# Performance work log

Measured on AMD Instinct MI355X. Metric: run time of the kernel, lower is better.

## Reference

```python
import jax, jax.numpy as jnp
import numpy as np

N = 20000   # nodes
E = 320000  # edges
D_IN = 256
D_OUT = 256


def setup_inputs() -> dict:
    key = jax.random.key(0)
    ks = jax.random.split(key, 12)
    s = 0.05
    return {
        "h": jax.random.normal(ks[0], (N, D_OUT), jnp.float32),
        "x": jax.random.normal(ks[1], (N, D_IN), jnp.float32),
        "pos": jax.random.normal(ks[2], (N, 3), jnp.float32),
        "W_fc": jax.random.normal(ks[3], (D_OUT, D_IN + D_OUT), jnp.float32) * s,
        "b_fc": jax.random.normal(ks[4], (D_OUT,), jnp.float32) * s,
        "W_conv": jax.random.normal(ks[5], (D_OUT, D_OUT), jnp.float32) * s,
        "W_ih": jax.random.normal(ks[6], (3 * D_OUT, D_OUT), jnp.float32) * s,
        "W_hh": jax.random.normal(ks[7], (3 * D_OUT, D_OUT), jnp.float32) * s,
        "b_ih": jax.random.normal(ks[8], (3 * D_OUT,), jnp.float32) * s,
        "b_hh": jax.random.normal(ks[9], (3 * D_OUT,), jnp.float32) * s,
        "edge_index_gate": jax.random.randint(ks[10], (2, E), 0, N, jnp.int64),
        "edge_index_cand": jax.random.randint(ks[11], (2, E), 0, N, jnp.int64),
    }


def reference(h, x, pos, W_fc, b_fc, W_conv, W_ih, W_hh, b_ih, b_hh,
              edge_index_gate, edge_index_cand):
    # fc + relu on concatenated [x, h]
    xh = jnp.concatenate([x, h], axis=-1)            # [N, in+out]
    xr = jax.nn.relu(xh @ W_fc.T + b_fc)             # [N, out]

    # GatedGraphConv, num_layers=1, aggr='add'
    m = xr @ W_conv                                  # [N, out]  (x @ weight[0])
    src, dst = edge_index_gate[0], edge_index_gate[1]
    agg = jax.ops.segment_sum(m[src], dst, num_segments=xr.shape[0])  # [N, out]

    # GRUCell(agg, xr)  (torch semantics: input=agg, hidden=xr)
    gi = agg @ W_ih.T + b_ih                         # [N, 3*out]
    gh = xr @ W_hh.T + b_hh                          # [N, 3*out]
    i_r, i_z, i_n = jnp.split(gi, 3, axis=-1)
    h_r, h_z, h_n = jnp.split(gh, 3, axis=-1)
    r = jax.nn.sigmoid(i_r + h_r)
    z = jax.nn.sigmoid(i_z + h_z)
    n = jnp.tanh(i_n + r * h_n)
    h_next = (1.0 - z) * n + z * xr
    return h_next
```

## Files before the change

kernel.cpp:

```cpp
#include <hip/hip_runtime.h>
#include <hip/hip_bf16.h>

#define N_NODES 20000
#define MPAD 20032
#define CAP 64

typedef __attribute__((ext_vector_type(8))) short short8;
typedef __attribute__((ext_vector_type(4))) float f32x4;

#define MFMA16(a,b,c) __builtin_amdgcn_mfma_f32_16x16x32_bf16(a,b,c,0,0,0)

#define FSW(r) (((r) & 3) ^ (((r) >> 2) & 3))

#define WAIT_BAR(NSTR) do { \
  asm volatile("s_waitcnt vmcnt(" NSTR ") lgkmcnt(0)" ::: "memory"); \
  __builtin_amdgcn_s_barrier(); \
  __builtin_amdgcn_sched_barrier(0); \
} while (0)
#define END_BAR() do { \
  __builtin_amdgcn_sched_barrier(0); \
  __builtin_amdgcn_s_barrier(); \
} while (0)

static __device__ __forceinline__ ushort f2bf(float f) {
  union { float f; uint u; } v; v.f = f;
  uint u = v.u;
  uint r = (u + 0x7FFFu + ((u >> 16) & 1u)) >> 16;
  return (ushort)r;
}
static __device__ __forceinline__ float bf2f(ushort s) {
  union { uint u; float f; } v; v.u = ((uint)s) << 16; return v.f;
}

typedef __attribute__((address_space(1))) const unsigned int guint;
typedef __attribute__((address_space(3))) unsigned int luint;
static __device__ __forceinline__ void gl2lds16(const void* g, void* l) {
  __builtin_amdgcn_global_load_lds((guint*)g, (luint*)l, 16, 0, 0);
}

static __device__ __forceinline__ void cvt8(const float* __restrict__ s, ushort* __restrict__ d) {
  float4 v0 = *(const float4*)s;
  float4 v1 = *(const float4*)(s + 4);
  union { ushort u[8]; uint4 v; } t;
  t.u[0]=f2bf(v0.x); t.u[1]=f2bf(v0.y); t.u[2]=f2bf(v0.z); t.u[3]=f2bf(v0.w);
  t.u[4]=f2bf(v1.x); t.u[5]=f2bf(v1.y); t.u[6]=f2bf(v1.z); t.u[7]=f2bf(v1.w);
  *(uint4*)d = t.v;
}
static __device__ __forceinline__ void cvt8_lds(const float* __restrict__ s, ushort* d) {
  float4 v0 = *(const float4*)s;
  float4 v1 = *(const float4*)(s + 4);
  union { ushort u[8]; uint4 v; } t;
  t.u[0]=f2bf(v0.x); t.u[1]=f2bf(v0.y); t.u[2]=f2bf(v0.z); t.u[3]=f2bf(v0.w);
  t.u[4]=f2bf(v1.x); t.u[5]=f2bf(v1.y); t.u[6]=f2bf(v1.z); t.u[7]=f2bf(v1.w);
  *(uint4*)d = t.v;
}

__global__ __launch_bounds__(256, 4) void k_mid(
    const float* __restrict__ x, const float* __restrict__ h,
    const float* __restrict__ Wfc, const float* __restrict__ bfc,
    ushort* __restrict__ AX,
    const float* __restrict__ Wih, const float* __restrict__ Wc,
    const float* __restrict__ Whh, ushort* __restrict__ Bg3,
    const int* __restrict__ eg, int* __restrict__ cnt, int* __restrict__ srcs) {
  __shared__ __attribute__((aligned(16))) ushort smem[8192];
  int bid = blockIdx.x;
  int t = threadIdx.x, w = t >> 6, l = t & 63;

  if (bid >= 1400) {
    int e = (bid - 1400) * 256 + t;
    if (e < 320000) {
      int d = eg[320000 + e];
      int slot = atomicAdd(&cnt[d], 1);
      if (slot < CAP) srcs[d * CAP + slot] = eg[e];
    }
    return;
  }

  if (bid >= 1304) {
    int i = (bid - 1304) * 256 + t;
    int row = i >> 5;
    int k0 = (i & 31) * 8;
    int g = row / 48, rem = row - g * 48;
    int p = rem >> 4, ci = rem & 15;
    int c = g * 16 + ci;
    cvt8(Whh + ((size_t)(p * 256 + c)) * 256 + k0, Bg3 + (size_t)row * 512 + 256 + k0);
    return;
  }

  if (bid >= 1256) {
    ushort* sA = smem;
    ushort* sB = smem + 2048;
    int wf = bid - 1256;
    int row0 = (wf % 12) * 64, col0 = (wf / 12) * 64;
    int wr = (w >> 1) * 32, wc = (w & 1) * 32;
    f32x4 acc[2][2] = {};
    for (int ks = 0; ks < 8; ++ks) {
      int k0 = ks * 32;
      {
        int r = t >> 2, wl = t & 3;
        int gw = wl ^ FSW(r);
        cvt8_lds(Wih + (size_t)(row0 + r) * 256 + k0 + gw * 8, &sA[r*32 + wl*8]);
        cvt8_lds(Wc  + (size_t)(col0 + r) * 256 + k0 + gw * 8, &sB[r*32 + wl*8]);
      }
      __syncthreads();
      short8 af[2], bfr[2];
      #pragma unroll
      for (int mi = 0; mi < 2; ++mi) {
        int r = wr + mi * 16 + (l & 15);
        af[mi] = *(short8*)&sA[r * 32 + (((l >> 4)) ^ FSW(r)) * 8];
      }
      #pragma unroll
      for (int ni = 0; ni < 2; ++ni) {
        int br = wc + ni * 16 + (l & 15);
        bfr[ni] = *(short8*)&sB[br * 32 + (((l >> 4)) ^ FSW(br)) * 8];
      }
      #pragma unroll
      for (int mi = 0; mi < 2; ++mi)
        #pragma unroll
        for (int ni = 0; ni < 2; ++ni)
          acc[mi][ni] = MFMA16(af[mi], bfr[ni], acc[mi][ni]);
      __syncthreads();
    }
    #pragma unroll
    for (int mi = 0; mi < 2; ++mi)
      #pragma unroll
      for (int ni = 0; ni < 2; ++ni)
        #pragma unroll
        for (int q = 0; q < 4; ++q) {
          int jj = row0 + wr + mi*16 + (l>>4)*4 + q;
          int tc = col0 + wc + ni*16 + (l&15);
          int p = jj >> 8, c = jj & 255;
          int brow = (c >> 4) * 48 + p * 16 + (c & 15);
          Bg3[(size_t)brow * 512 + tc] = f2bf(acc[mi][ni][q]);
        }
    return;
  }

  ushort* sA = smem;
  ushort* sB = smem + 4096;
  int wk = (bid & 7) * 157 + (bid >> 3);
  int panel = wk >> 2, ch = wk & 3;
  if (panel >= 313) return;
  int row0 = panel * 64, col0 = ch * 64;
  int wr = (w >> 1) * 32, wc = (w & 1) * 32;

  f32x4 acc[2][2] = {};
  for (int ks = 0; ks < 8; ++ks) {
    int k0 = ks * 64;
    const float* Af = (ks < 4) ? x : h;
    int ka = k0 & 255;
    #pragma unroll
    for (int j = 0; j < 2; ++j) {
      int ci = t + j * 256;
      int r = ci >> 3, wl = ci & 7;
      int gw = wl ^ (r & 7);
      int gr = row0 + r; if (gr > N_NODES - 1) gr = N_NODES - 1;
      cvt8_lds(Af + (size_t)gr * 256 + ka + gw * 8, &sA[r*64 + wl*8]);
    }
    #pragma unroll
    for (int j = 0; j < 2; ++j) {
      int ci = t + j * 256;
      int r = ci >> 3, wl = ci & 7;
      int gw = wl ^ (r & 7);
      cvt8_lds(Wfc + (size_t)(col0 + r) * 512 + k0 + gw * 8, &sB[r*64 + wl*8]);
    }
    __syncthreads();
    #pragma unroll
    for (int j = 0; j < 2; ++j) {
      short8 af[2], bfr[2];
      #pragma unroll
      for (int mi = 0; mi < 2; ++mi) {
        int r = wr + mi * 16 + (l & 15);
        af[mi] = *(short8*)&sA[r * 64 + ((j * 4 + (l >> 4)) ^ (r & 7)) * 8];
      }
      #pragma unroll
      for (int ni = 0; ni < 2; ++ni) {
        int br = wc + ni * 16 + (l & 15);
        bfr[ni] = *(short8*)&sB[br * 64 + ((j * 4 + (l >> 4)) ^ (br & 7)) * 8];
      }
      #pragma unroll
      for (int mi = 0; mi < 2; ++mi)
        #pragma unroll
        for (int ni = 0; ni < 2; ++ni)
          acc[mi][ni] = MFMA16(af[mi], bfr[ni], acc[mi][ni]);
    }
    __syncthreads();
  }
  #pragma unroll
  for (int mi = 0; mi < 2; ++mi)
    #pragma unroll
    for (int ni = 0; ni < 2; ++ni)
      #pragma unroll
      for (int q = 0; q < 4; ++q) {
        int r = row0 + wr + mi*16 + (l>>4)*4 + q;
        int c = col0 + wc + ni*16 + (l&15);
        if (r < N_NODES) {
          float v = acc[mi][ni][q] + bfc[c];
          v = v > 0.f ? v : 0.f;
          AX[(size_t)r * 512 + 256 + c] = f2bf(v);
        }
      }
}

__global__ __launch_bounds__(256) void k_aggS(
    const int* __restrict__ cnt, const int* __restrict__ srcs,
    ushort* __restrict__ AX) {
  int node = blockIdx.x * 8 + (threadIdx.x >> 5);
  if (node >= N_NODES) return;
  int lane = threadIdx.x & 31;
  const int* bkt = srcs + node * CAP;
  int n = cnt[node]; if (n > CAP) n = CAP;
  float a[8] = {};
  int i = 0;
  for (; i + 4 <= n; i += 4) {
    uint4 v0 = *(const uint4*)(AX + (size_t)bkt[i  ] * 512 + 256 + lane * 8);
    uint4 v1 = *(const uint4*)(AX + (size_t)bkt[i+1] * 512 + 256 + lane * 8);
    uint4 v2 = *(const uint4*)(AX + (size_t)bkt[i+2] * 512 + 256 + lane * 8);
    uint4 v3 = *(const uint4*)(AX + (size_t)bkt[i+3] * 512 + 256 + lane * 8);
    const ushort* p0 = (const ushort*)&v0; const ushort* p1 = (const ushort*)&v1;
    const ushort* p2 = (const ushort*)&v2; const ushort* p3 = (const ushort*)&v3;
    #pragma unroll
    for (int j = 0; j < 8; j++) a[j] += (bf2f(p0[j]) + bf2f(p1[j])) + (bf2f(p2[j]) + bf2f(p3[j]));
  }
  for (; i < n; ++i) {
    uint4 v0 = *(const uint4*)(AX + (size_t)bkt[i] * 512 + 256 + lane * 8);
    const ushort* p0 = (const ushort*)&v0;
    #pragma unroll
    for (int j = 0; j < 8; j++) a[j] += bf2f(p0[j]);
  }
  union { ushort s[8]; uint4 v; } o;
  #pragma unroll
  for (int j = 0; j < 8; j++) o.s[j] = f2bf(a[j]);
  *(uint4*)(AX + (size_t)node * 512 + lane * 8) = o.v;
}

static __device__ __forceinline__ void gru3_stage(
    const ushort* __restrict__ AX, const ushort* __restrict__ Bg3,
    ushort* sA, ushort* sB, int row0, int bro, int w, int l, int ks) {
  int k0 = ks * 64;
  #pragma unroll
  for (int j = 0; j < 2; ++j) {
    int rb = w * 16 + j * 8;
    int r = rb + (l >> 3);
    int gw = (l & 7) ^ (r & 7);
    gl2lds16(AX + (size_t)(row0 + r) * 512 + k0 + gw * 8, (char*)sA + (size_t)rb * 128);
  }
  #pragma unroll
  for (int j = 0; j < 6; ++j) {
    int rb = j * 32 + w * 8;
    int r = rb + (l >> 3);
    int gw = (l & 7) ^ (r & 7);
    gl2lds16(Bg3 + (size_t)(bro + r) * 512 + k0 + gw * 8, (char*)sB + (size_t)rb * 128);
  }
}

template<int PN>
static __device__ __forceinline__ void gru3_compute(
    const ushort* sA, const ushort* sB, int w, int l, f32x4 (&acc)[4][4]) {
  __builtin_amdgcn_s_setprio(1);
  #pragma unroll
  for (int j = 0; j < 2; ++j) {
    short8 af[4], bfr[3];
    #pragma unroll
    for (int mi = 0; mi < 4; ++mi) {
      int r = mi * 16 + (l & 15);
      af[mi] = *(const short8*)&sA[r * 64 + ((j * 4 + (l >> 4)) ^ (r & 7)) * 8];
    }
    #pragma unroll
    for (int p = 0; p < 3; ++p) {
      int br = w * 48 + p * 16 + (l & 15);
      bfr[p] = *(const short8*)&sB[br * 64 + ((j * 4 + (l >> 4)) ^ (br & 7)) * 8];
    }
    #pragma unroll
    for (int mi = 0; mi < 4; ++mi) {
      acc[mi][0]  = MFMA16(af[mi], bfr[0], acc[mi][0]);
      acc[mi][1]  = MFMA16(af[mi], bfr[1], acc[mi][1]);
      acc[mi][PN] = MFMA16(af[mi], bfr[2], acc[mi][PN]);
    }
  }
  __builtin_amdgcn_s_setprio(0);
}

__global__ __launch_bounds__(256, 2) void k_gru3(
    const ushort* __restrict__ AX, const ushort* __restrict__ Bg3,
    const float* __restrict__ bih, const float* __restrict__ bhh,
    float* __restrict__ out) {
  __shared__ __attribute__((aligned(16))) ushort smem[2 * 16384];
  ushort* sA0 = smem;
  ushort* sB0 = smem + 4096;
  ushort* sA1 = smem + 16384;
  ushort* sB1 = smem + 20480;
  int bid = blockIdx.x;
  int wk = (bid & 7) * 157 + (bid >> 3);
  int panel = wk >> 2, ch = wk & 3;
  if (panel >= 313) return;
  int row0 = panel * 64;
  int bro = ch * 192;
  int t = threadIdx.x, w = t >> 6, l = t & 63;

  gru3_stage(AX, Bg3, sA0, sB0, row0, bro, w, l, 0);
  __syncthreads();

  f32x4 acc[4][4] = {};
  #pragma unroll
  for (int ks = 0; ks < 8; ++ks) {
    ushort* cA = (ks & 1) ? sA1 : sA0;
    ushort* cB = (ks & 1) ? sB1 : sB0;
    ushort* nA = (ks & 1) ? sA0 : sA1;
    ushort* nB = (ks & 1) ? sB0 : sB1;
    if (ks < 7) gru3_stage(AX, Bg3, nA, nB, row0, bro, w, l, ks + 1);
    if (ks < 7) WAIT_BAR("8");
    else        WAIT_BAR("0");
    if (ks < 4) gru3_compute<2>(cA, cB, w, l, acc);
    else        gru3_compute<3>(cA, cB, w, l, acc);
    END_BAR();
  }

  int c = ch * 64 + w * 16 + (l & 15);
  float br_ = bih[c] + bhh[c];
  float bz_ = bih[256 + c] + bhh[256 + c];
  float bi_ = bih[512 + c];
  float bh_ = bhh[512 + c];
  #pragma unroll
  for (int mi = 0; mi < 4; ++mi)
    #pragma unroll
    for (int q = 0; q < 4; ++q) {
      int r = row0 + mi*16 + (l>>4)*4 + q;
      if (r < N_NODES) {
        float rg = 1.f / (1.f + __expf(-(acc[mi][0][q] + br_)));
        float zg = 1.f / (1.f + __expf(-(acc[mi][1][q] + bz_)));
        float ng = tanhf((acc[mi][2][q] + bi_) + rg * (acc[mi][3][q] + bh_));
        float xv = bf2f(AX[(size_t)r * 512 + 256 + c]);
        out[(size_t)r * 256 + c] = (1.f - zg) * ng + zg * xv;
      }
    }
}

extern "C" void kernel_launch(void* const* d_in, const int* in_sizes, int n_in,
                              void* d_out, int out_size, void* d_ws, size_t ws_size,
                              hipStream_t stream) {
  const float* h   = (const float*)d_in[0];
  const float* x   = (const float*)d_in[1];
  const float* Wfc = (const float*)d_in[3];
  const float* bfc = (const float*)d_in[4];
  const float* Wc  = (const float*)d_in[5];
  const float* Wih = (const float*)d_in[6];
  const float* Whh = (const float*)d_in[7];
  const float* bih = (const float*)d_in[8];
  const float* bhh = (const float*)d_in[9];
  const int*   eg  = (const int*)d_in[10];
  float* out = (float*)d_out;

  char* ws = (char*)d_ws;
  ushort* AX   = (ushort*)(ws);
  ushort* Bg3  = (ushort*)(ws + 20512768);
  int*    cnt    = (int*)(ws + 21299200);
  int*    srcs   = (int*)(ws + 21379200);

  hipMemsetAsync(cnt, 0, (size_t)N_NODES * 4, stream);

  k_mid<<<2650, 256, 0, stream>>>(x, h, Wfc, bfc, AX, Wih, Wc, Whh, Bg3, eg, cnt, srcs);

  k_aggS<<<(N_NODES + 7) / 8, 256, 0, stream>>>(cnt, srcs, AX);

  k_gru3<<<1256, 256, 0, stream>>>(AX, Bg3, bih, bhh, out);
}
```

Baseline: 88.78 us.

## Pre-convert W_fc to bf16 and double-buffer the fc GEMM with wider tiles

A new small kernel converts W_fc to bf16 once, so the fc GEMM can stream B tiles straight into LDS with global_load_lds instead of converting fp32 per block. The fc GEMM tile grows from 64x64 to 64x128 and uses double-buffered LDS: the next A tile is loaded into registers and the next B tile into the other buffer while the current tile's MFMAs run. This halves the number of fc blocks and hides load latency, at the cost of more LDS per block (occupancy hint lowered to 3) and an extra kernel launch.

Measured after the change: 93.32 us. +5.1%, slower.

```diff
diff --git a/kernel.cpp b/kernel.cpp
--- a/kernel.cpp
+++ b/kernel.cpp
@@ -46,28 +46,32 @@
   t.u[4]=f2bf(v1.x); t.u[5]=f2bf(v1.y); t.u[6]=f2bf(v1.z); t.u[7]=f2bf(v1.w);
   *(uint4*)d = t.v;
 }
-static __device__ __forceinline__ void cvt8_lds(const float* __restrict__ s, ushort* d) {
-  float4 v0 = *(const float4*)s;
-  float4 v1 = *(const float4*)(s + 4);
+static __device__ __forceinline__ void pack8(float4 v0, float4 v1, ushort* d) {
   union { ushort u[8]; uint4 v; } t;
   t.u[0]=f2bf(v0.x); t.u[1]=f2bf(v0.y); t.u[2]=f2bf(v0.z); t.u[3]=f2bf(v0.w);
   t.u[4]=f2bf(v1.x); t.u[5]=f2bf(v1.y); t.u[6]=f2bf(v1.z); t.u[7]=f2bf(v1.w);
   *(uint4*)d = t.v;
 }
 
-__global__ __launch_bounds__(256, 4) void k_mid(
+__global__ __launch_bounds__(256) void k_prep0(
+    const float* __restrict__ Wfc, ushort* __restrict__ WfcB) {
+  int i = blockIdx.x * 256 + threadIdx.x;
+  if (i < 16384) cvt8(Wfc + i * 8, WfcB + i * 8);
+}
+
+__global__ __launch_bounds__(256, 3) void k_mid(
     const float* __restrict__ x, const float* __restrict__ h,
-    const float* __restrict__ Wfc, const float* __restrict__ bfc,
+    const ushort* __restrict__ WfcB, const float* __restrict__ bfc,
     ushort* __restrict__ AX,
     const float* __restrict__ Wih, const float* __restrict__ Wc,
     const float* __restrict__ Whh, ushort* __restrict__ Bg3,
     const int* __restrict__ eg, int* __restrict__ cnt, int* __restrict__ srcs) {
-  __shared__ __attribute__((aligned(16))) ushort smem[8192];
+  __shared__ __attribute__((aligned(16))) ushort smem[24576];
   int bid = blockIdx.x;
   int t = threadIdx.x, w = t >> 6, l = t & 63;
 
-  if (bid >= 1400) {
-    int e = (bid - 1400) * 256 + t;
+  if (bid >= 776) {
+    int e = (bid - 776) * 256 + t;
     if (e < 320000) {
       int d = eg[320000 + e];
       int slot = atomicAdd(&cnt[d], 1);
@@ -76,8 +80,8 @@
     return;
   }
 
-  if (bid >= 1304) {
-    int i = (bid - 1304) * 256 + t;
+  if (bid >= 680) {
+    int i = (bid - 680) * 256 + t;
     int row = i >> 5;
     int k0 = (i & 31) * 8;
     int g = row / 48, rem = row - g * 48;
@@ -87,10 +91,10 @@
     return;
   }
 
-  if (bid >= 1256) {
+  if (bid >= 632) {
     ushort* sA = smem;
     ushort* sB = smem + 2048;
-    int wf = bid - 1256;
+    int wf = bid - 632;
     int row0 = (wf % 12) * 64, col0 = (wf / 12) * 64;
     int wr = (w >> 1) * 32, wc = (w & 1) * 32;
     f32x4 acc[2][2] = {};
@@ -99,8 +103,8 @@
       {
         int r = t >> 2, wl = t & 3;
         int gw = wl ^ FSW(r);
-        cvt8_lds(Wih + (size_t)(row0 + r) * 256 + k0 + gw * 8, &sA[r*32 + wl*8]);
-        cvt8_lds(Wc  + (size_t)(col0 + r) * 256 + k0 + gw * 8, &sB[r*32 + wl*8]);
+        cvt8(Wih + (size_t)(row0 + r) * 256 + k0 + gw * 8, &sA[r*32 + wl*8]);
+        cvt8(Wc  + (size_t)(col0 + r) * 256 + k0 + gw * 8, &sB[r*32 + wl*8]);
       }
       __syncthreads();
       short8 af[2], bfr[2];
@@ -136,64 +140,91 @@
     return;
   }
 
-  ushort* sA = smem;
-  ushort* sB = smem + 4096;
-  int wk = (bid & 7) * 157 + (bid >> 3);
-  int panel = wk >> 2, ch = wk & 3;
+  ushort* A0 = smem;
+  ushort* B0 = smem + 4096;
+  ushort* A1 = smem + 12288;
+  ushort* B1 = smem + 16384;
+  int wk = (bid & 7) * 79 + (bid >> 3);
+  int panel = wk >> 1, ch = wk & 1;
   if (panel >= 313) return;
-  int row0 = panel * 64, col0 = ch * 64;
-  int wr = (w >> 1) * 32, wc = (w & 1) * 32;
-
-  f32x4 acc[2][2] = {};
+  int row0 = panel * 64, col0 = ch * 128;
+
+  int r0c = t >> 3,        wl0 = t & 7,        gw0 = wl0 ^ (r0c & 7);
+  int r1c = (t + 256) >> 3, wl1 = t & 7,       gw1 = wl1 ^ (r1c & 7);
+  int gr0 = row0 + r0c; if (gr0 > N_NODES - 1) gr0 = N_NODES - 1;
+  int gr1 = row0 + r1c; if (gr1 > N_NODES - 1) gr1 = N_NODES - 1;
+
+  {
+    const float* Af = x;
+    cvt8(Af + (size_t)gr0 * 256 + 0 + gw0 * 8, &A0[r0c * 64 + wl0 * 8]);
+    cvt8(Af + (size_t)gr1 * 256 + 0 + gw1 * 8, &A0[r1c * 64 + wl1 * 8]);
+    #pragma unroll
+    for (int j = 0; j < 4; ++j) {
+      int rb = j * 32 + w * 8;
+      int r = rb + (l >> 3);
+      int gw = (l & 7) ^ (r & 7);
+      gl2lds16(WfcB + (size_t)(col0 + r) * 512 + 0 + gw * 8, (char*)B0 + (size_t)rb * 128);
+    }
+  }
+  __syncthreads();
+
+  f32x4 acc[4][2] = {};
+  #pragma unroll
   for (int ks = 0; ks < 8; ++ks) {
-    int k0 = ks * 64;
-    const float* Af = (ks < 4) ? x : h;
-    int ka = k0 & 255;
+    ushort* cA = (ks & 1) ? A1 : A0;
+    ushort* cB = (ks & 1) ? B1 : B0;
+    ushort* nA = (ks & 1) ? A0 : A1;
+    ushort* nB = (ks & 1) ? B0 : B1;
+    float4 a0, a1, a2, a3;
+    if (ks < 7) {
+      const float* Af = (ks + 1 < 4) ? x : h;
+      int ka = ((ks + 1) * 64) & 255;
+      const float* pa0 = Af + (size_t)gr0 * 256 + ka + gw0 * 8;
+      const float* pa1 = Af + (size_t)gr1 * 256 + ka + gw1 * 8;
+      a0 = *(const float4*)pa0; a1 = *(const float4*)(pa0 + 4);
+      a2 = *(const float4*)pa1; a3 = *(const float4*)(pa1 + 4);
+      int k0 = (ks + 1) * 64;
+      #pragma unroll
+      for (int j = 0; j < 4; ++j) {
+        int rb = j * 32 + w * 8;
+        int r = rb + (l >> 3);
+        int gw = (l & 7) ^ (r & 7);
+        gl2lds16(WfcB + (size_t)(col0 + r) * 512 + k0 + gw * 8, (char*)nB + (size_t)rb * 128);
+      }
+    }
     #pragma unroll
     for (int j = 0; j < 2; ++j) {
-      int ci = t + j * 256;
-      int r = ci >> 3, wl = ci & 7;
-      int gw = wl ^ (r & 7);
-      int gr = row0 + r; if (gr > N_NODES - 1) gr = N_NODES - 1;
-      cvt8_lds(Af + (size_t)gr * 256 + ka + gw * 8, &sA[r*64 + wl*8]);
-    }
-    #pragma unroll
-    for (int j = 0; j < 2; ++j) {
-      int ci = t + j * 256;
-      int r = ci >> 3, wl = ci & 7;
-      int gw = wl ^ (r & 7);
-      cvt8_lds(Wfc + (size_t)(col0 + r) * 512 + k0 + gw * 8, &sB[r*64 + wl*8]);
-    }
-    __syncthreads();
-    #pragma unroll
-    for (int j = 0; j < 2; ++j) {
-      short8 af[2], bfr[2];
-      #pragma unroll
-      for (int mi = 0; mi < 2; ++mi) {
-        int r = wr + mi * 16 + (l & 15);
-        af[mi] = *(short8*)&sA[r * 64 + ((j * 4 + (l >> 4)) ^ (r & 7)) * 8];
+      short8 af[4], bfr[2];
+      #pragma unroll
+      for (int mi = 0; mi < 4; ++mi) {
+        int r = mi * 16 + (l & 15);
+        af[mi] = *(short8*)&cA[r * 64 + ((j * 4 + (l >> 4)) ^ (r & 7)) * 8];
       }
       #pragma unroll
       for (int ni = 0; ni < 2; ++ni) {
-        int br = wc + ni * 16 + (l & 15);
-        bfr[ni] = *(short8*)&sB[br * 64 + ((j * 4 + (l >> 4)) ^ (br & 7)) * 8];
-      }
-      #pragma unroll
-      for (int mi = 0; mi < 2; ++mi)
+        int br = w * 32 + ni * 16 + (l & 15);
+        bfr[ni] = *(short8*)&cB[br * 64 + ((j * 4 + (l >> 4)) ^ (br & 7)) * 8];
+      }
+      #pragma unroll
+      for (int mi = 0; mi < 4; ++mi)
         #pragma unroll
         for (int ni = 0; ni < 2; ++ni)
           acc[mi][ni] = MFMA16(af[mi], bfr[ni], acc[mi][ni]);
     }
+    if (ks < 7) {
+      pack8(a0, a1, &nA[r0c * 64 + wl0 * 8]);
+      pack8(a2, a3, &nA[r1c * 64 + wl1 * 8]);
+    }
     __syncthreads();
   }
   #pragma unroll
-  for (int mi = 0; mi < 2; ++mi)
+  for (int mi = 0; mi < 4; ++mi)
     #pragma unroll
     for (int ni = 0; ni < 2; ++ni)
       #pragma unroll
       for (int q = 0; q < 4; ++q) {
-        int r = row0 + wr + mi*16 + (l>>4)*4 + q;
-        int c = col0 + wc + ni*16 + (l&15);
+        int r = row0 + mi*16 + (l>>4)*4 + q;
+        int c = col0 + w*32 + ni*16 + (l&15);
         if (r < N_NODES) {
           float v = acc[mi][ni][q] + bfc[c];
           v = v > 0.f ? v : 0.f;
@@ -354,12 +385,14 @@
   char* ws = (char*)d_ws;
   ushort* AX   = (ushort*)(ws);
   ushort* Bg3  = (ushort*)(ws + 20512768);
-  int*    cnt    = (int*)(ws + 21299200);
-  int*    srcs   = (int*)(ws + 21379200);
+  ushort* WfcB = (ushort*)(ws + 21299200);
+  int*    cnt    = (int*)(ws + 21561344);
+  int*    srcs   = (int*)(ws + 21641344);
 
   hipMemsetAsync(cnt, 0, (size_t)N_NODES * 4, stream);
-
-  k_mid<<<2650, 256, 0, stream>>>(x, h, Wfc, bfc, AX, Wih, Wc, Whh, Bg3, eg, cnt, srcs);
+  k_prep0<<<64, 256, 0, stream>>>(Wfc, WfcB);
+
+  k_mid<<<2026, 256, 0, stream>>>(x, h, WfcB, bfc, AX, Wih, Wc, Whh, Bg3, eg, cnt, srcs);
 
   k_aggS<<<(N_NODES + 7) / 8, 256, 0, stream>>>(cnt, srcs, AX);
 
```

## Pre-convert inputs to bf16 and double-buffer fc GEMM with async LDS loads

Applied to the files above, without the earlier changes.

Adds a pre-pass kernel that converts x, h and W_fc to bf16 into a concatenated XH buffer and runs the edge bucketing. The fc GEMM now streams bf16 tiles straight into LDS with global_load_lds, using two LDS buffers so the next k-slice loads while the current one computes. The goal is to drop per-tile fp32 conversion from the GEMM inner loop and hide load latency. The cost is an extra kernel launch plus a full bf16 copy of the inputs written to and re-read from global memory, and doubled LDS use per block, which may lower occupancy.

New measurement: 104.5 us. 1.18x slower.

```diff
diff --git a/kernel.cpp b/kernel.cpp
--- a/kernel.cpp
+++ b/kernel.cpp
@@ -46,28 +46,17 @@
   t.u[4]=f2bf(v1.x); t.u[5]=f2bf(v1.y); t.u[6]=f2bf(v1.z); t.u[7]=f2bf(v1.w);
   *(uint4*)d = t.v;
 }
-static __device__ __forceinline__ void cvt8_lds(const float* __restrict__ s, ushort* d) {
-  float4 v0 = *(const float4*)s;
-  float4 v1 = *(const float4*)(s + 4);
-  union { ushort u[8]; uint4 v; } t;
-  t.u[0]=f2bf(v0.x); t.u[1]=f2bf(v0.y); t.u[2]=f2bf(v0.z); t.u[3]=f2bf(v0.w);
-  t.u[4]=f2bf(v1.x); t.u[5]=f2bf(v1.y); t.u[6]=f2bf(v1.z); t.u[7]=f2bf(v1.w);
-  *(uint4*)d = t.v;
-}
-
-__global__ __launch_bounds__(256, 4) void k_mid(
+
+__global__ __launch_bounds__(256) void k_pre(
     const float* __restrict__ x, const float* __restrict__ h,
-    const float* __restrict__ Wfc, const float* __restrict__ bfc,
-    ushort* __restrict__ AX,
-    const float* __restrict__ Wih, const float* __restrict__ Wc,
-    const float* __restrict__ Whh, ushort* __restrict__ Bg3,
+    const float* __restrict__ Wfc,
+    ushort* __restrict__ XH, ushort* __restrict__ WfcB,
     const int* __restrict__ eg, int* __restrict__ cnt, int* __restrict__ srcs) {
-  __shared__ __attribute__((aligned(16))) ushort smem[8192];
   int bid = blockIdx.x;
-  int t = threadIdx.x, w = t >> 6, l = t & 63;
-
-  if (bid >= 1400) {
-    int e = (bid - 1400) * 256 + t;
+  int t = threadIdx.x;
+
+  if (bid >= 2568) {
+    int e = (bid - 2568) * 256 + t;
     if (e < 320000) {
       int d = eg[320000 + e];
       int slot = atomicAdd(&cnt[d], 1);
@@ -75,6 +64,32 @@
     }
     return;
   }
+  if (bid >= 2504) {
+    int i = (bid - 2504) * 256 + t;
+    cvt8(Wfc + i * 8, WfcB + i * 8);
+    return;
+  }
+  #pragma unroll
+  for (int j = 0; j < 2; ++j) {
+    int ci = bid * 512 + t + j * 256;
+    int row = ci >> 6, wi = ci & 63;
+    if (row < N_NODES) {
+      if (wi < 32) cvt8(x + (size_t)row * 256 + wi * 8,        XH + (size_t)row * 512 + wi * 8);
+      else         cvt8(h + (size_t)row * 256 + (wi - 32) * 8, XH + (size_t)row * 512 + wi * 8);
+    } else {
+      *(uint4*)&XH[(size_t)row * 512 + wi * 8] = make_uint4(0, 0, 0, 0);
+    }
+  }
+}
+
+__global__ __launch_bounds__(256, 4) void k_mid(
+    const ushort* __restrict__ XH, const ushort* __restrict__ WfcB,
+    const float* __restrict__ bfc, ushort* __restrict__ AX,
+    const float* __restrict__ Wih, const float* __restrict__ Wc,
+    const float* __restrict__ Whh, ushort* __restrict__ Bg3) {
+  __shared__ __attribute__((aligned(16))) ushort smem[16384];
+  int bid = blockIdx.x;
+  int t = threadIdx.x, w = t >> 6, l = t & 63;
 
   if (bid >= 1304) {
     int i = (bid - 1304) * 256 + t;
@@ -99,8 +114,8 @@
       {
         int r = t >> 2, wl = t & 3;
         int gw = wl ^ FSW(r);
-        cvt8_lds(Wih + (size_t)(row0 + r) * 256 + k0 + gw * 8, &sA[r*32 + wl*8]);
-        cvt8_lds(Wc  + (size_t)(col0 + r) * 256 + k0 + gw * 8, &sB[r*32 + wl*8]);
+        cvt8(Wih + (size_t)(row0 + r) * 256 + k0 + gw * 8, &sA[r*32 + wl*8]);
+        cvt8(Wc  + (size_t)(col0 + r) * 256 + k0 + gw * 8, &sB[r*32 + wl*8]);
       }
       __syncthreads();
       short8 af[2], bfr[2];
@@ -136,47 +151,60 @@
     return;
   }
 
-  ushort* sA = smem;
-  ushort* sB = smem + 4096;
+  ushort* A0 = smem;
+  ushort* B0 = smem + 4096;
+  ushort* A1 = smem + 8192;
+  ushort* B1 = smem + 12288;
   int wk = (bid & 7) * 157 + (bid >> 3);
   int panel = wk >> 2, ch = wk & 3;
   if (panel >= 313) return;
   int row0 = panel * 64, col0 = ch * 64;
   int wr = (w >> 1) * 32, wc = (w & 1) * 32;
 
+  #define FC_STAGE(sa, sb, KS) do { \
+    int k0_ = (KS) * 64; \
+    _Pragma("unroll") \
+    for (int j = 0; j < 2; ++j) { \
+      int rb = w * 16 + j * 8; \
+      int r = rb + (l >> 3); \
+      int gw = (l & 7) ^ (r & 7); \
+      gl2lds16(XH + (size_t)(row0 + r) * 512 + k0_ + gw * 8, (char*)(sa) + (size_t)rb * 128); \
+    } \
+    _Pragma("unroll") \
+    for (int j = 0; j < 2; ++j) { \
+      int rb = w * 16 + j * 8; \
+      int r = rb + (l >> 3); \
+      int gw = (l & 7) ^ (r & 7); \
+      gl2lds16(WfcB + (size_t)(col0 + r) * 512 + k0_ + gw * 8, (char*)(sb) + (size_t)rb * 128); \
+    } \
+  } while (0)
+
+  FC_STAGE(A0, B0, 0);
+  __syncthreads();
+
   f32x4 acc[2][2] = {};
+  #pragma unroll
   for (int ks = 0; ks < 8; ++ks) {
-    int k0 = ks * 64;
-    const float* Af = (ks < 4) ? x : h;
-    int ka = k0 & 255;
-    #pragma unroll
-    for (int j = 0; j < 2; ++j) {
-      int ci = t + j * 256;
-      int r = ci >> 3, wl = ci & 7;
-      int gw = wl ^ (r & 7);
-      int gr = row0 + r; if (gr > N_NODES - 1) gr = N_NODES - 1;
-      cvt8_lds(Af + (size_t)gr * 256 + ka + gw * 8, &sA[r*64 + wl*8]);
-    }
-    #pragma unroll
-    for (int j = 0; j < 2; ++j) {
-      int ci = t + j * 256;
-      int r = ci >> 3, wl = ci & 7;
-      int gw = wl ^ (r & 7);
-      cvt8_lds(Wfc + (size_t)(col0 + r) * 512 + k0 + gw * 8, &sB[r*64 + wl*8]);
-    }
-    __syncthreads();
+    ushort* cA = (ks & 1) ? A1 : A0;
+    ushort* cB = (ks & 1) ? B1 : B0;
+    ushort* nA = (ks & 1) ? A0 : A1;
+    ushort* nB = (ks & 1) ? B0 : B1;
+    if (ks < 7) FC_STAGE(nA, nB, ks + 1);
+    if (ks < 7) WAIT_BAR("4");
+    else        WAIT_BAR("0");
+    __builtin_amdgcn_s_setprio(1);
     #pragma unroll
     for (int j = 0; j < 2; ++j) {
       short8 af[2], bfr[2];
       #pragma unroll
       for (int mi = 0; mi < 2; ++mi) {
         int r = wr + mi * 16 + (l & 15);
-        af[mi] = *(short8*)&sA[r * 64 + ((j * 4 + (l >> 4)) ^ (r & 7)) * 8];
+        af[mi] = *(short8*)&cA[r * 64 + ((j * 4 + (l >> 4)) ^ (r & 7)) * 8];
       }
       #pragma unroll
       for (int ni = 0; ni < 2; ++ni) {
         int br = wc + ni * 16 + (l & 15);
-        bfr[ni] = *(short8*)&sB[br * 64 + ((j * 4 + (l >> 4)) ^ (br & 7)) * 8];
+        bfr[ni] = *(short8*)&cB[br * 64 + ((j * 4 + (l >> 4)) ^ (br & 7)) * 8];
       }
       #pragma unroll
       for (int mi = 0; mi < 2; ++mi)
@@ -184,8 +212,10 @@
         for (int ni = 0; ni < 2; ++ni)
           acc[mi][ni] = MFMA16(af[mi], bfr[ni], acc[mi][ni]);
     }
-    __syncthreads();
-  }
+    __builtin_amdgcn_s_setprio(0);
+    END_BAR();
+  }
+  #undef FC_STAGE
   #pragma unroll
   for (int mi = 0; mi < 2; ++mi)
     #pragma unroll
@@ -353,13 +383,17 @@
 
   char* ws = (char*)d_ws;
   ushort* AX   = (ushort*)(ws);
-  ushort* Bg3  = (ushort*)(ws + 20512768);
-  int*    cnt    = (int*)(ws + 21299200);
-  int*    srcs   = (int*)(ws + 21379200);
+  ushort* XH   = (ushort*)(ws + 20512768);
+  ushort* Bg3  = (ushort*)(ws + 41025536);
+  ushort* WfcB = (ushort*)(ws + 41811968);
+  int*    cnt    = (int*)(ws + 42074112);
+  int*    srcs   = (int*)(ws + 42154112);
 
   hipMemsetAsync(cnt, 0, (size_t)N_NODES * 4, stream);
 
-  k_mid<<<2650, 256, 0, stream>>>(x, h, Wfc, bfc, AX, Wih, Wc, Whh, Bg3, eg, cnt, srcs);
+  k_pre<<<3818, 256, 0, stream>>>(x, h, Wfc, XH, WfcB, eg, cnt, srcs);
+
+  k_mid<<<1400, 256, 0, stream>>>(XH, WfcB, bfc, AX, Wih, Wc, Whh, Bg3);
 
   k_aggS<<<(N_NODES + 7) / 8, 256, 0, stream>>>(cnt, srcs, AX);
 
```
